# Performance work log

Measured on AMD Instinct MI355X. Metric: run time of the kernel, lower is better.

Reference implementation:

```python
import jax, jax.numpy as jnp
import numpy as np

N_NODES = 100000
N_EDGES = 640000
D_FEAT = 128
UNITS = 128


def setup_inputs() -> dict:
    key = jax.random.key(0)
    k1, k2, k3, k4, k5 = jax.random.split(key, 5)
    X = jax.random.normal(k1, (N_NODES, D_FEAT), dtype=jnp.float32)
    ref_A = jax.random.randint(k2, (N_EDGES,), 0, N_NODES, dtype=jnp.int32)
    ref_B = jax.random.randint(k3, (N_EDGES,), 0, N_NODES, dtype=jnp.int32)
    # GlorotUniform-style params (scale approximated; exact init irrelevant for math)
    limit_w = np.sqrt(6.0 / (D_FEAT + UNITS)).astype(np.float32)
    w = jax.random.uniform(k4, (D_FEAT, UNITS), minval=-limit_w, maxval=limit_w, dtype=jnp.float32)
    b = jax.random.uniform(k5, (UNITS,), minval=-0.1, maxval=0.1, dtype=jnp.float32)
    return {"X": X, "ref_A": ref_A, "ref_B": ref_B, "w": w, "b": b}


def reference(X, ref_A, ref_B, w, b):
    # c.convolution: gather source-node features along edges, scatter-add to
    # destination nodes (sum aggregation over incoming messages).
    msgs = X[ref_A]                                        # [E, D]
    agg = jax.ops.segment_sum(msgs, ref_B, num_segments=X.shape[0])  # [N, D]
    out = agg @ w + b                                      # [N, units]
    return out
```

## Files before the change

### kernel.cpp

```cpp
#include <hip/hip_runtime.h>
#include <hip/hip_bf16.h>

typedef short s16x8 __attribute__((ext_vector_type(8)));
typedef float f32x4 __attribute__((ext_vector_type(4)));

#define CAPN 32

static __device__ inline unsigned short f2bf(float f) {
    __hip_bfloat16 h = __float2bfloat16(f);
    return *reinterpret_cast<unsigned short*>(&h);
}

__global__ __launch_bounds__(256) void prep_kernel(
    const float* __restrict__ X, const float* __restrict__ w,
    unsigned int* __restrict__ Xb, unsigned short* __restrict__ wT,
    int* __restrict__ cnt, int N, int nx)
{
    int i = blockIdx.x * 256 + threadIdx.x;
    if (i < nx) {
        int n = i >> 6, c = i & 63;
        float x0 = X[(size_t)n * 128 + c];
        float x1 = X[(size_t)n * 128 + c + 64];
        Xb[i] = (unsigned int)f2bf(x0) | ((unsigned int)f2bf(x1) << 16);
    }
    if (i < 16384) {
        int n = i >> 7, k = i & 127;
        wT[i] = f2bf(w[k * 128 + n]);
    }
    if (i < N) cnt[i] = 0;
}

__global__ __launch_bounds__(256) void fill_kernel(
    const int* __restrict__ A, const int* __restrict__ B,
    int* __restrict__ cnt, unsigned int* __restrict__ entries, int E)
{
    int e = blockIdx.x * 256 + threadIdx.x;
    if (e < E) {
        int d = B[e];
        int pos = atomicAdd(&cnt[d], 1);
        if (pos < CAPN)
            entries[(size_t)d * CAPN + pos] = (unsigned int)A[e];
    }
}

__global__ __launch_bounds__(1024) void aggemm_kernel(
    const unsigned int* __restrict__ Xb, const int* __restrict__ cnt,
    const unsigned int* __restrict__ entries, const unsigned short* __restrict__ wT,
    const float* __restrict__ b, float* __restrict__ out, int N)
{
    __shared__ unsigned short atile[64 * 136];

    const int tid  = threadIdx.x;
    const int u    = tid >> 6;
    const int lane = tid & 63;
    const int m    = lane & 15;
    const int q    = lane >> 4;
    const int row0 = blockIdx.x * 64;

    #pragma unroll 1
    for (int t = 0; t < 4; ++t) {
        const int lrow = u * 4 + t;
        const int node = row0 + lrow;
        float ax = 0.f, ay = 0.f;
        if (node < N) {
            int deg = cnt[node];
            if (deg > CAPN) deg = CAPN;
            const unsigned int* eb = entries + (size_t)node * CAPN;
            unsigned int idx_l = (lane < deg) ? eb[lane] : 0u;
            int j = 0;
            for (; j + 3 < deg; j += 4) {
                unsigned int s0 = __shfl(idx_l, j);
                unsigned int s1 = __shfl(idx_l, j + 1);
                unsigned int s2 = __shfl(idx_l, j + 2);
                unsigned int s3 = __shfl(idx_l, j + 3);
                unsigned int p0 = Xb[(size_t)s0 * 64 + lane];
                unsigned int p1 = Xb[(size_t)s1 * 64 + lane];
                unsigned int p2 = Xb[(size_t)s2 * 64 + lane];
                unsigned int p3 = Xb[(size_t)s3 * 64 + lane];
                ax += __uint_as_float(p0 << 16) + __uint_as_float(p1 << 16)
                    + __uint_as_float(p2 << 16) + __uint_as_float(p3 << 16);
                ay += __uint_as_float(p0 & 0xFFFF0000u) + __uint_as_float(p1 & 0xFFFF0000u)
                    + __uint_as_float(p2 & 0xFFFF0000u) + __uint_as_float(p3 & 0xFFFF0000u);
            }
            for (; j < deg; ++j) {
                unsigned int s0 = __shfl(idx_l, j);
                unsigned int p0 = Xb[(size_t)s0 * 64 + lane];
                ax += __uint_as_float(p0 << 16);
                ay += __uint_as_float(p0 & 0xFFFF0000u);
            }
        }
        atile[lrow * 136 + lane]      = f2bf(ax);
        atile[lrow * 136 + 64 + lane] = f2bf(ay);
    }
    __syncthreads();

    if (u < 4) {
        const unsigned short* arow = &atile[(u * 16 + m) * 136];
        f32x4 acc[8] = {};
        #pragma unroll
        for (int s = 0; s < 4; ++s) {
            s16x8 a = *(const s16x8*)&arow[s * 32 + q * 8];
            #pragma unroll
            for (int c = 0; c < 8; ++c) {
                s16x8 bf = *(const s16x8*)&wT[(size_t)(c * 16 + m) * 128 + s * 32 + q * 8];
                acc[c] = __builtin_amdgcn_mfma_f32_16x16x32_bf16(a, bf, acc[c], 0, 0, 0);
            }
        }
        const int r0g = row0 + u * 16 + q * 4;
        #pragma unroll
        for (int c = 0; c < 8; ++c) {
            int col = c * 16 + m;
            float bias = b[col];
            #pragma unroll
            for (int r = 0; r < 4; ++r) {
                int row = r0g + r;
                if (row < N)
                    out[(size_t)row * 128 + col] = acc[c][r] + bias;
            }
        }
    }
}

extern "C" void kernel_launch(void* const* d_in, const int* in_sizes, int n_in,
                              void* d_out, int out_size, void* d_ws, size_t ws_size,
                              hipStream_t stream) {
    const float* X = (const float*)d_in[0];
    const int*   A = (const int*)d_in[1];
    const int*   B = (const int*)d_in[2];
    const float* w = (const float*)d_in[3];
    const float* b = (const float*)d_in[4];
    float* out = (float*)d_out;

    const int N = in_sizes[0] / 128;
    const int E = in_sizes[1];
    const int nx = N * 64;

    char* wsb = (char*)d_ws;
    size_t off = 0;
    int* cnt = (int*)(wsb + off); off += (size_t)4 * N;
    off = (off + 255) & ~(size_t)255;
    unsigned short* wT = (unsigned short*)(wsb + off); off += 32768;
    unsigned int* Xb = (unsigned int*)(wsb + off); off += (size_t)nx * 4;
    unsigned int* entries = (unsigned int*)(wsb + off);

    prep_kernel<<<(nx + 255) / 256, 256, 0, stream>>>(X, w, Xb, wT, cnt, N, nx);
    fill_kernel<<<(E + 255) / 256, 256, 0, stream>>>(A, B, cnt, entries, E);
    aggemm_kernel<<<(N + 63) / 64, 1024, 0, stream>>>(Xb, cnt, entries, wT, b, out, N);
}
```

Measured before the change: 231.7 us.

## Fuse prep and fill kernels; gather in padded 8-wide chunks via zero row

Merges the bf16 conversion kernel and the edge bucketing kernel into one launch, moving the count reset to a memset beforehand. Appends a zero row to the packed feature buffer so the gather loop can always issue 8 independent loads per chunk, padding out-of-range slots with the zero row instead of using a remainder loop. This aims to cut launch overhead and raise memory-level parallelism in the gather. The cost is extra wasted loads for low-degree nodes, though they all hit the same cached zero row.

```diff
diff --git a/kernel.cpp b/kernel.cpp
--- a/kernel.cpp
+++ b/kernel.cpp
@@ -11,35 +11,33 @@
     return *reinterpret_cast<unsigned short*>(&h);
 }
 
-__global__ __launch_bounds__(256) void prep_kernel(
+__global__ __launch_bounds__(256) void prep_fill_kernel(
     const float* __restrict__ X, const float* __restrict__ w,
+    const int* __restrict__ A, const int* __restrict__ B,
     unsigned int* __restrict__ Xb, unsigned short* __restrict__ wT,
-    int* __restrict__ cnt, int N, int nx)
+    int* __restrict__ cnt, unsigned int* __restrict__ entries,
+    int N, int nx2, int E)
 {
     int i = blockIdx.x * 256 + threadIdx.x;
-    if (i < nx) {
+    if (i < nx2) {
         int n = i >> 6, c = i & 63;
-        float x0 = X[(size_t)n * 128 + c];
-        float x1 = X[(size_t)n * 128 + c + 64];
-        Xb[i] = (unsigned int)f2bf(x0) | ((unsigned int)f2bf(x1) << 16);
+        unsigned int pk = 0u;
+        if (n < N) {
+            float x0 = X[(size_t)n * 128 + c];
+            float x1 = X[(size_t)n * 128 + c + 64];
+            pk = (unsigned int)f2bf(x0) | ((unsigned int)f2bf(x1) << 16);
+        }
+        Xb[i] = pk;
     }
     if (i < 16384) {
         int n = i >> 7, k = i & 127;
         wT[i] = f2bf(w[k * 128 + n]);
     }
-    if (i < N) cnt[i] = 0;
-}
-
-__global__ __launch_bounds__(256) void fill_kernel(
-    const int* __restrict__ A, const int* __restrict__ B,
-    int* __restrict__ cnt, unsigned int* __restrict__ entries, int E)
-{
-    int e = blockIdx.x * 256 + threadIdx.x;
-    if (e < E) {
-        int d = B[e];
+    if (i < E) {
+        int d = B[i];
         int pos = atomicAdd(&cnt[d], 1);
         if (pos < CAPN)
-            entries[(size_t)d * CAPN + pos] = (unsigned int)A[e];
+            entries[(size_t)d * CAPN + pos] = (unsigned int)A[i];
     }
 }
 
@@ -66,27 +64,23 @@
             int deg = cnt[node];
             if (deg > CAPN) deg = CAPN;
             const unsigned int* eb = entries + (size_t)node * CAPN;
-            unsigned int idx_l = (lane < deg) ? eb[lane] : 0u;
-            int j = 0;
-            for (; j + 3 < deg; j += 4) {
-                unsigned int s0 = __shfl(idx_l, j);
-                unsigned int s1 = __shfl(idx_l, j + 1);
-                unsigned int s2 = __shfl(idx_l, j + 2);
-                unsigned int s3 = __shfl(idx_l, j + 3);
-                unsigned int p0 = Xb[(size_t)s0 * 64 + lane];
-                unsigned int p1 = Xb[(size_t)s1 * 64 + lane];
-                unsigned int p2 = Xb[(size_t)s2 * 64 + lane];
-                unsigned int p3 = Xb[(size_t)s3 * 64 + lane];
-                ax += __uint_as_float(p0 << 16) + __uint_as_float(p1 << 16)
-                    + __uint_as_float(p2 << 16) + __uint_as_float(p3 << 16);
-                ay += __uint_as_float(p0 & 0xFFFF0000u) + __uint_as_float(p1 & 0xFFFF0000u)
-                    + __uint_as_float(p2 & 0xFFFF0000u) + __uint_as_float(p3 & 0xFFFF0000u);
-            }
-            for (; j < deg; ++j) {
-                unsigned int s0 = __shfl(idx_l, j);
-                unsigned int p0 = Xb[(size_t)s0 * 64 + lane];
-                ax += __uint_as_float(p0 << 16);
-                ay += __uint_as_float(p0 & 0xFFFF0000u);
+            int idx_l = (lane < deg) ? (int)eb[lane] : 0;
+            const int chunks = (deg + 7) >> 3;
+            #pragma unroll 1
+            for (int ch = 0; ch < chunks; ++ch) {
+                const int base = ch * 8;
+                unsigned int p[8];
+                #pragma unroll
+                for (int j = 0; j < 8; ++j) {
+                    int sl = base + j;
+                    int s = (sl < deg) ? __shfl(idx_l, sl) : N;
+                    p[j] = Xb[(size_t)s * 64 + lane];
+                }
+                #pragma unroll
+                for (int j = 0; j < 8; ++j) {
+                    ax += __uint_as_float(p[j] << 16);
+                    ay += __uint_as_float(p[j] & 0xFFFF0000u);
+                }
             }
         }
         atile[lrow * 136 + lane]      = f2bf(ax);
@@ -133,17 +127,18 @@
 
     const int N = in_sizes[0] / 128;
     const int E = in_sizes[1];
-    const int nx = N * 64;
+    const int nx2 = (N + 1) * 64;
 
     char* wsb = (char*)d_ws;
     size_t off = 0;
     int* cnt = (int*)(wsb + off); off += (size_t)4 * N;
     off = (off + 255) & ~(size_t)255;
     unsigned short* wT = (unsigned short*)(wsb + off); off += 32768;
-    unsigned int* Xb = (unsigned int*)(wsb + off); off += (size_t)nx * 4;
+    unsigned int* Xb = (unsigned int*)(wsb + off); off += (size_t)nx2 * 4;
     unsigned int* entries = (unsigned int*)(wsb + off);
 
-    prep_kernel<<<(nx + 255) / 256, 256, 0, stream>>>(X, w, Xb, wT, cnt, N, nx);
-    fill_kernel<<<(E + 255) / 256, 256, 0, stream>>>(A, B, cnt, entries, E);
+    hipMemsetAsync(cnt, 0, (size_t)4 * N, stream);
+    prep_fill_kernel<<<(nx2 + 255) / 256, 256, 0, stream>>>(
+        X, w, A, B, Xb, wT, cnt, entries, N, nx2, E);
     aggemm_kernel<<<(N + 63) / 64, 1024, 0, stream>>>(Xb, cnt, entries, wT, b, out, N);
 }
```

Result: faster. 221.6 us (-4.4%).
